# Optimization experiments

Measured on AMD Instinct MI355X. Metric: run time of the kernel, lower is better.

Reference implementation:

```python
import jax, jax.numpy as jnp
import numpy as np

# BEV grid config from __init__ defaults
X0, XS, BX = -50.0, 0.5, 200
Y0, YS, BY = -50.0, 0.5, 200
Z0, Z1, BZ = -10.0, 10.0, 20


def setup_inputs() -> dict:
    key = jax.random.key(0)
    k1, k2, k3 = jax.random.split(key, 3)
    B, N, D, H, W, C = 2, 6, 41, 28, 50, 64
    # ego-frame 3D points; range slightly larger than BEV bounds so some are invalid
    geometry = jax.random.uniform(k1, (B, N, D, H, W, 3), minval=-60.0, maxval=60.0)
    features = jax.random.normal(k2, (B, N, C, H, W), dtype=jnp.float32)
    # depth distribution over D bins per pixel
    depth_probs = jax.nn.softmax(jax.random.normal(k3, (B, N, D, H, W)), axis=2)
    return {"geometry": geometry, "features": features, "depth_probs": depth_probs}


def _pool_one(geom, feat, depth):
    # geom: [N, D, H, W, 3], feat: [N, C, H, W], depth: [N, D, H, W]
    x, y, z = geom[..., 0], geom[..., 1], geom[..., 2]
    # torch .long() truncates toward zero -> jnp.trunc
    xi = jnp.trunc((x - X0) / XS).astype(jnp.int32)
    yi = jnp.trunc((y - Y0) / YS).astype(jnp.int32)
    zi = jnp.trunc((z - Z0) / (Z1 - Z0) * BZ).astype(jnp.int32)
    valid = (xi >= 0) & (xi < BX) & (yi >= 0) & (yi < BY) & (zi >= 0) & (zi < BZ)
    lin = jnp.where(valid, (zi * BY + yi) * BX + xi, 0).reshape(-1)   # [P]
    w = jnp.where(valid, depth, 0.0).reshape(-1)                      # [P]
    N, C, H, W = feat.shape
    D = depth.shape[1]
    # expand per-pixel features across depth bins: [N, D, H, W, C] -> [P, C]
    feat_pts = jnp.broadcast_to(
        feat.transpose(0, 2, 3, 1)[:, None], (N, D, H, W, C)
    ).reshape(-1, C)
    vals = feat_pts * w[:, None]                                      # [P, C]
    voxel = jnp.zeros((BZ * BY * BX, C), dtype=vals.dtype).at[lin].add(vals)
    voxel = voxel.reshape(BZ, BY, BX, C)
    bev = voxel.max(axis=0)                                           # [BY, BX, C]
    return bev.transpose(2, 0, 1)                                     # [C, BY, BX]


def reference(geometry, features, depth_probs):
    # -> (B, C, bev_y, bev_x)
    return jax.vmap(_pool_one)(geometry, features, depth_probs)
```

## Files before the change

kernel.cpp:

```cpp
#include <hip/hip_runtime.h>
#include <hip/hip_bf16.h>

#define CC 64
#define HW 1400
#define DHW 57400
#define NPTS 688800
#define NCOL 80000
#define KCAP 24

#define OFF_CNT    0
#define OFF_BUCKET 320000
#define OFF_FEATT  15680000

__global__ __launch_bounds__(256) void k0_init_transpose(const float* __restrict__ feat,
                                                         float* __restrict__ feat_t,
                                                         int* __restrict__ cnt) {
    int gid = blockIdx.x * 256 + threadIdx.x;
    for (int i = gid; i < NCOL; i += gridDim.x * 256) cnt[i] = 0;

    __shared__ float tile[64][65];
    int bn  = blockIdx.x / 22;
    int t   = blockIdx.x % 22;
    int hw0 = t * 64;
    int wv   = threadIdx.x >> 6;
    int lane = threadIdx.x & 63;

    const float* src = feat + bn * CC * HW;
    #pragma unroll
    for (int i = 0; i < 16; ++i) {
        int c = wv * 16 + i, hw = hw0 + lane;
        if (hw < HW) tile[c][lane] = src[c * HW + hw];
    }
    __syncthreads();
    float* dst = feat_t + bn * HW * CC;
    #pragma unroll
    for (int i = 0; i < 16; ++i) {
        int hwl = wv * 16 + i, hw = hw0 + hwl;
        if (hw < HW) dst[hw * CC + lane] = tile[lane][hwl];
    }
}

__global__ __launch_bounds__(256) void k1_bin(const float* __restrict__ geom,
                                              const float* __restrict__ depth,
                                              int* __restrict__ cnt,
                                              int2* __restrict__ bucket) {
    int pt = blockIdx.x * 256 + threadIdx.x;
    if (pt >= NPTS) return;

    float x = geom[3 * pt + 0];
    float y = geom[3 * pt + 1];
    float z = geom[3 * pt + 2];

    float fx = (x + 50.0f) / 0.5f;
    float fy = (y + 50.0f) / 0.5f;
    float fz = (z + 10.0f) / 20.0f * 20.0f;
    int xi = (int)fx, yi = (int)fy, zi = (int)fz;

    bool valid = (xi >= 0) & (xi < 200) & (yi >= 0) & (yi < 200) & (zi >= 0) & (zi < 20);
    if (!valid) return;

    int bn = pt / DHW;
    int hw = (pt - bn * DHW) % HW;
    int b  = bn / 6;
    int col = b * 40000 + yi * 200 + xi;

    int idx = atomicAdd(&cnt[col], 1);
    if (idx < KCAP)
        bucket[(size_t)col * KCAP + idx] =
            make_int2(__float_as_int(depth[pt]), ((bn * HW + hw) << 5) | zi);
}

__global__ __launch_bounds__(1024) void k2_pool(const int* __restrict__ cnt,
                                                const int2* __restrict__ bucket,
                                                const float* __restrict__ feat_t,
                                                float* __restrict__ out) {
    __shared__ int2  recs[64 * KCAP];
    __shared__ int   cnts[64];
    __shared__ float buf[64][65];
    int tid  = threadIdx.x;
    int wv   = tid >> 6;
    int lane = tid & 63;
    int b    = blockIdx.x / 625;
    int yx0  = (blockIdx.x % 625) * 64;
    int colBase = b * 40000 + yx0;

    const int2* gsrc = bucket + (size_t)colBase * KCAP;
    recs[tid] = gsrc[tid];
    if (tid < 64 * KCAP - 1024) recs[1024 + tid] = gsrc[1024 + tid];
    if (tid < 64) cnts[tid] = cnt[colBase + tid];
    __syncthreads();

    #pragma unroll
    for (int j = 0; j < 4; ++j) {
        int colLocal = wv * 4 + j;
        int k = cnts[colLocal];
        if (k > KCAP) k = KCAP;
        const int2* rec = &recs[colLocal * KCAP];

        float m = 0.0f;
        unsigned handled = 0;
        for (int i = 0; i < k; ++i) {
            if ((handled >> i) & 1) continue;
            int2 ri = rec[i];
            int zi  = ri.y & 31;
            float s = __int_as_float(ri.x) * feat_t[(ri.y >> 5) * CC + lane];
            for (int t = i + 1; t < k; ++t) {
                int2 rt = rec[t];
                if (((handled >> t) & 1) == 0 && (rt.y & 31) == zi) {
                    s += __int_as_float(rt.x) * feat_t[(rt.y >> 5) * CC + lane];
                    handled |= 1u << t;
                }
            }
            m = fmaxf(m, s);
        }
        buf[colLocal][lane] = m;
    }
    __syncthreads();
    #pragma unroll
    for (int i = 0; i < 4; ++i) {
        int c = wv * 4 + i;
        out[((size_t)b * CC + c) * 40000 + yx0 + lane] = buf[lane][c];
    }
}

extern "C" void kernel_launch(void* const* d_in, const int* in_sizes, int n_in,
                              void* d_out, int out_size, void* d_ws, size_t ws_size,
                              hipStream_t stream) {
    const float* geom  = (const float*)d_in[0];
    const float* feat  = (const float*)d_in[1];
    const float* depth = (const float*)d_in[2];
    float* out = (float*)d_out;

    char* ws = (char*)d_ws;
    int*   cntp   = (int*)(ws + OFF_CNT);
    int2*  bucket = (int2*)(ws + OFF_BUCKET);
    float* feat_t = (float*)(ws + OFF_FEATT);

    hipLaunchKernelGGL(k0_init_transpose, dim3(264),  dim3(256),  0, stream, feat, feat_t, cntp);
    hipLaunchKernelGGL(k1_bin,            dim3(2691), dim3(256),  0, stream, geom, depth, cntp, bucket);
    hipLaunchKernelGGL(k2_pool,           dim3(1250), dim3(1024), 0, stream, cntp, bucket, feat_t, out);
}
```

Measured before the change: 40.84 us.

## Bucket points per tile, store features as bf16, and fuse prep kernels

Binning now groups valid points by 64-column tile instead of by column. The pool kernel re-distributes those records into per-column shared buckets with shared-memory atomics, so it reads only the live records instead of a sparse fixed-capacity array. The transposed features are stored in bf16, which halves gather traffic at some cost in precision. The transpose and binning kernels are merged into one launch, and a memset clears the tile counters.

```diff
diff --git a/kernel.cpp b/kernel.cpp
--- a/kernel.cpp
+++ b/kernel.cpp
@@ -5,46 +5,50 @@
 #define HW 1400
 #define DHW 57400
 #define NPTS 688800
-#define NCOL 80000
+#define NTILE 1250
+#define TCAP 256
 #define KCAP 24
 
-#define OFF_CNT    0
-#define OFF_BUCKET 320000
-#define OFF_FEATT  15680000
+#define OFF_TCNT   0
+#define OFF_BUCKET 5120
+#define OFF_FEATT  2565120
 
-__global__ __launch_bounds__(256) void k0_init_transpose(const float* __restrict__ feat,
-                                                         float* __restrict__ feat_t,
-                                                         int* __restrict__ cnt) {
-    int gid = blockIdx.x * 256 + threadIdx.x;
-    for (int i = gid; i < NCOL; i += gridDim.x * 256) cnt[i] = 0;
-
-    __shared__ float tile[64][65];
-    int bn  = blockIdx.x / 22;
-    int t   = blockIdx.x % 22;
-    int hw0 = t * 64;
-    int wv   = threadIdx.x >> 6;
-    int lane = threadIdx.x & 63;
-
-    const float* src = feat + bn * CC * HW;
-    #pragma unroll
-    for (int i = 0; i < 16; ++i) {
-        int c = wv * 16 + i, hw = hw0 + lane;
-        if (hw < HW) tile[c][lane] = src[c * HW + hw];
-    }
-    __syncthreads();
-    float* dst = feat_t + bn * HW * CC;
-    #pragma unroll
-    for (int i = 0; i < 16; ++i) {
-        int hwl = wv * 16 + i, hw = hw0 + hwl;
-        if (hw < HW) dst[hw * CC + lane] = tile[lane][hwl];
-    }
+static __device__ __forceinline__ unsigned short f32_to_bf16_rne(float v) {
+    unsigned int u = __float_as_uint(v);
+    unsigned int r = u + 0x7fffu + ((u >> 16) & 1u);
+    return (unsigned short)(r >> 16);
 }
 
-__global__ __launch_bounds__(256) void k1_bin(const float* __restrict__ geom,
-                                              const float* __restrict__ depth,
-                                              int* __restrict__ cnt,
-                                              int2* __restrict__ bucket) {
-    int pt = blockIdx.x * 256 + threadIdx.x;
+__global__ __launch_bounds__(256) void k01_prep(const float* __restrict__ feat,
+                                                const float* __restrict__ geom,
+                                                const float* __restrict__ depth,
+                                                unsigned short* __restrict__ feat_t,
+                                                int* __restrict__ tcnt,
+                                                int2* __restrict__ bucket) {
+    int bid = blockIdx.x;
+    if (bid < 264) {
+        __shared__ float tile[64][65];
+        int bn  = bid / 22;
+        int hw0 = (bid % 22) * 64;
+        int wv   = threadIdx.x >> 6;
+        int lane = threadIdx.x & 63;
+        const float* src = feat + bn * CC * HW;
+        #pragma unroll
+        for (int i = 0; i < 16; ++i) {
+            int c = wv * 16 + i, hw = hw0 + lane;
+            if (hw < HW) tile[c][lane] = src[c * HW + hw];
+        }
+        __syncthreads();
+        unsigned short* dst = feat_t + bn * HW * CC;
+        #pragma unroll
+        for (int i = 0; i < 16; ++i) {
+            int hwl = wv * 16 + i, hw = hw0 + hwl;
+            if (hw < HW) dst[hw * CC + lane] = f32_to_bf16_rne(tile[lane][hwl]);
+        }
+        return;
+    }
+
+    int pt = (bid - 264) * 256 + threadIdx.x;
     if (pt >= NPTS) return;
 
     float x = geom[3 * pt + 0];
@@ -59,55 +63,66 @@
     bool valid = (xi >= 0) & (xi < 200) & (yi >= 0) & (yi < 200) & (zi >= 0) & (zi < 20);
     if (!valid) return;
 
-    int bn = pt / DHW;
-    int hw = (pt - bn * DHW) % HW;
-    int b  = bn / 6;
-    int col = b * 40000 + yi * 200 + xi;
+    int bn  = pt / DHW;
+    int hw  = (pt - bn * DHW) % HW;
+    int b   = bn / 6;
+    int yx  = yi * 200 + xi;
+    int tl  = b * 625 + (yx >> 6);
+    int pix = bn * HW + hw;
 
-    int idx = atomicAdd(&cnt[col], 1);
-    if (idx < KCAP)
-        bucket[(size_t)col * KCAP + idx] =
-            make_int2(__float_as_int(depth[pt]), ((bn * HW + hw) << 5) | zi);
+    int idx = atomicAdd(&tcnt[tl], 1);
+    if (idx < TCAP)
+        bucket[tl * TCAP + idx] =
+            make_int2(__float_as_int(depth[pt]), (pix << 11) | ((yx & 63) << 5) | zi);
 }
 
-__global__ __launch_bounds__(1024) void k2_pool(const int* __restrict__ cnt,
+__global__ __launch_bounds__(1024) void k2_pool(const int* __restrict__ tcnt,
                                                 const int2* __restrict__ bucket,
-                                                const float* __restrict__ feat_t,
+                                                const unsigned short* __restrict__ feat_t,
                                                 float* __restrict__ out) {
-    __shared__ int2  recs[64 * KCAP];
-    __shared__ int   cnts[64];
+    __shared__ int2  lrec[64][KCAP];
+    __shared__ int   lcnt[64];
     __shared__ float buf[64][65];
     int tid  = threadIdx.x;
     int wv   = tid >> 6;
     int lane = tid & 63;
     int b    = blockIdx.x / 625;
     int yx0  = (blockIdx.x % 625) * 64;
-    int colBase = b * 40000 + yx0;
 
-    const int2* gsrc = bucket + (size_t)colBase * KCAP;
-    recs[tid] = gsrc[tid];
-    if (tid < 64 * KCAP - 1024) recs[1024 + tid] = gsrc[1024 + tid];
-    if (tid < 64) cnts[tid] = cnt[colBase + tid];
+    if (tid < 64) lcnt[tid] = 0;
+    __syncthreads();
+
+    int cnt = tcnt[blockIdx.x];
+    if (cnt > TCAP) cnt = TCAP;
+    if (tid < cnt) {
+        int2 r = bucket[blockIdx.x * TCAP + tid];
+        int  c = (r.y >> 5) & 63;
+        int  s = atomicAdd(&lcnt[c], 1);
+        if (s < KCAP) lrec[c][s] = r;
+    }
     __syncthreads();
 
     #pragma unroll
     for (int j = 0; j < 4; ++j) {
         int colLocal = wv * 4 + j;
-        int k = cnts[colLocal];
+        int k = lcnt[colLocal];
         if (k > KCAP) k = KCAP;
-        const int2* rec = &recs[colLocal * KCAP];
 
         float m = 0.0f;
         unsigned handled = 0;
         for (int i = 0; i < k; ++i) {
             if ((handled >> i) & 1) continue;
-            int2 ri = rec[i];
+            int2 ri = lrec[colLocal][i];
             int zi  = ri.y & 31;
-            float s = __int_as_float(ri.x) * feat_t[(ri.y >> 5) * CC + lane];
+            unsigned pix = ((unsigned)ri.y) >> 11;
+            float f = __uint_as_float((unsigned)feat_t[pix * CC + lane] << 16);
+            float s = __int_as_float(ri.x) * f;
             for (int t = i + 1; t < k; ++t) {
-                int2 rt = rec[t];
+                int2 rt = lrec[colLocal][t];
                 if (((handled >> t) & 1) == 0 && (rt.y & 31) == zi) {
-                    s += __int_as_float(rt.x) * feat_t[(rt.y >> 5) * CC + lane];
+                    unsigned pt2 = ((unsigned)rt.y) >> 11;
+                    float f2 = __uint_as_float((unsigned)feat_t[pt2 * CC + lane] << 16);
+                    s += __int_as_float(rt.x) * f2;
                     handled |= 1u << t;
                 }
             }
@@ -132,11 +147,11 @@
     float* out = (float*)d_out;
 
     char* ws = (char*)d_ws;
-    int*   cntp   = (int*)(ws + OFF_CNT);
-    int2*  bucket = (int2*)(ws + OFF_BUCKET);
-    float* feat_t = (float*)(ws + OFF_FEATT);
+    int*            tcnt   = (int*)(ws + OFF_TCNT);
+    int2*           bucket = (int2*)(ws + OFF_BUCKET);
+    unsigned short* feat_t = (unsigned short*)(ws + OFF_FEATT);
 
-    hipLaunchKernelGGL(k0_init_transpose, dim3(264),  dim3(256),  0, stream, feat, feat_t, cntp);
-    hipLaunchKernelGGL(k1_bin,            dim3(2691), dim3(256),  0, stream, geom, depth, cntp, bucket);
-    hipLaunchKernelGGL(k2_pool,           dim3(1250), dim3(1024), 0, stream, cntp, bucket, feat_t, out);
+    hipMemsetAsync(tcnt, 0, NTILE * sizeof(int), stream);
+    hipLaunchKernelGGL(k01_prep, dim3(2955), dim3(256),  0, stream, feat, geom, depth, feat_t, tcnt, bucket);
+    hipLaunchKernelGGL(k2_pool,  dim3(1250), dim3(1024), 0, stream, tcnt, bucket, feat_t, out);
 }
```

Result: slower. 67.40 us (+65.0%).
